# Kernel tuning notes

Hardware: AMD Instinct MI355X
Metric: run time of the kernel (lower is better)

## Reference

```python
import jax, jax.numpy as jnp
import numpy as np

B, S, H, NH = 2, 2048, 1024, 16
HD = H // NH


def setup_inputs() -> dict:
    key = jax.random.key(0)
    ks = jax.random.split(key, 14)
    lim = 1.0 / np.sqrt(H)  # torch Linear default init range
    def lin(ka, kb):
        W = jax.random.uniform(ka, (H, H), jnp.float32, -lim, lim)
        b = jax.random.uniform(kb, (H,), jnp.float32, -lim, lim)
        return W, b
    Wq, bq = lin(ks[0], ks[1])
    Wk, bk = lin(ks[2], ks[3])
    Wv, bv = lin(ks[4], ks[5])
    Wo, bo = lin(ks[6], ks[7])
    return {
        "query": jax.random.normal(ks[8], (B, S, H), jnp.float32),
        "key": jax.random.normal(ks[9], (B, S, H), jnp.float32),
        "value": jax.random.normal(ks[10], (B, S, H), jnp.float32),
        "attn_mask": jax.random.randint(ks[11], (B, S, S), 0, 2).astype(bool),
        "relative_time": jax.random.normal(ks[12], (B, 1, S, S), jnp.float32),
        "Wq": Wq, "bq": bq, "Wk": Wk, "bk": bk,
        "Wv": Wv, "bv": bv, "Wo": Wo, "bo": bo,
    }


def reference(query, key, value, attn_mask, relative_time,
              Wq, bq, Wk, bk, Wv, bv, Wo, bo):
    Bq, Sq, _ = query.shape
    Skv = key.shape[1]
    # projections (torch Linear: x @ W^T + b)
    Q = (query @ Wq.T + bq).reshape(Bq, Sq, NH, HD).transpose(0, 2, 1, 3)
    K = (key @ Wk.T + bk).reshape(Bq, Skv, NH, HD).transpose(0, 2, 1, 3)
    V = (value @ Wv.T + bv).reshape(Bq, Skv, NH, HD).transpose(0, 2, 1, 3)
    scale = HD ** (-0.5)
    # NOTE: bias added BEFORE scaling, matching the original (non-standard)
    scores = jnp.einsum("bhqd,bhkd->bhqk", Q, K)
    scores = (scores + relative_time) * scale
    scores = jnp.where(attn_mask[:, None, :, :], scores, -jnp.inf)
    attn = jax.nn.softmax(scores.astype(jnp.float32), axis=-1).astype(scores.dtype)
    attn = jnp.nan_to_num(attn, nan=0.0)
    # dropout is identity in eval mode (dropout_rate applied only when training)
    out = jnp.einsum("bhqk,bhkd->bhqd", attn, V)
    out = out.transpose(0, 2, 1, 3).reshape(Bq, Sq, H)
    return out @ Wo.T + bo
```

## Files before the change

### kernel.cpp

```cpp
#include <hip/hip_runtime.h>
#include <hip/hip_bf16.h>

constexpr int BATCH = 2, SEQ = 2048, HDIM = 1024, NHEADS = 16, HEADD = 64;
constexpr int MROWS = BATCH * SEQ;
constexpr float QSCALE = 0.18033688011112042f;

typedef short short8 __attribute__((ext_vector_type(8)));
typedef float f32x4  __attribute__((ext_vector_type(4)));

static __device__ __forceinline__ short f2bf(float f) {
    __hip_bfloat16 h = __float2bfloat16(f);
    return *reinterpret_cast<short*>(&h);
}

static __device__ __forceinline__ void gload_lds16(const void* g, void* l) {
    __builtin_amdgcn_global_load_lds(
        (const __attribute__((address_space(1))) unsigned int*)g,
        (__attribute__((address_space(3))) unsigned int*)l, 16, 0, 0);
}

__global__ void cvt_qkv_kernel(const float* __restrict__ q, const float* __restrict__ k,
                               const float* __restrict__ v, short* __restrict__ xq,
                               short* __restrict__ xk, short* __restrict__ xv, int n4) {
    int i = blockIdx.x * blockDim.x + threadIdx.x;
    const int stride = gridDim.x * blockDim.x;
    for (; i < 3 * n4; i += stride) {
        const float* in; short* out; int j = i;
        if (j >= 2 * n4)      { in = v; out = xv; j -= 2 * n4; }
        else if (j >= n4)     { in = k; out = xk; j -= n4; }
        else                  { in = q; out = xq; }
        const float4 val = reinterpret_cast<const float4*>(in)[j];
        short4 o;
        o.x = f2bf(val.x); o.y = f2bf(val.y); o.z = f2bf(val.z); o.w = f2bf(val.w);
        reinterpret_cast<short4*>(out)[j] = o;
    }
}

__global__ void cvt_w4_kernel(const float* __restrict__ w0, const float* __restrict__ w1,
                              const float* __restrict__ w2, const float* __restrict__ w3,
                              short* __restrict__ o0, short* __restrict__ o1,
                              short* __restrict__ o2, short* __restrict__ o3, int n4) {
    int i = blockIdx.x * blockDim.x + threadIdx.x;
    const int stride = gridDim.x * blockDim.x;
    for (; i < 4 * n4; i += stride) {
        const float* in; short* out; int j = i;
        if (j >= 3 * n4)      { in = w3; out = o3; j -= 3 * n4; }
        else if (j >= 2 * n4) { in = w2; out = o2; j -= 2 * n4; }
        else if (j >= n4)     { in = w1; out = o1; j -= n4; }
        else                  { in = w0; out = o0; }
        const float4 val = reinterpret_cast<const float4*>(in)[j];
        short4 o;
        o.x = f2bf(val.x); o.y = f2bf(val.y); o.z = f2bf(val.z); o.w = f2bf(val.w);
        reinterpret_cast<short4*>(out)[j] = o;
    }
}

__global__ void detect_mask_kernel(const unsigned int* __restrict__ m, int* flag) {
    const int tid = threadIdx.x;
    int gt1 = 0, isf = 0;
    for (int i = 0; i < 4; ++i) {
        unsigned int wv = m[tid + 256 * i];
        if (wv > 1u) gt1 = 1;
        if (wv == 0x3F800000u) isf = 1;
    }
    __shared__ int s_gt1, s_isf;
    if (tid == 0) { s_gt1 = 0; s_isf = 0; }
    __syncthreads();
    if (gt1) atomicOr(&s_gt1, 1);
    if (isf) atomicOr(&s_isf, 1);
    __syncthreads();
    if (tid == 0) flag[0] = s_gt1 ? (s_isf ? 2 : 1) : 0;
}

__global__ void fuse_rel_kernel(const float* __restrict__ rel, const void* __restrict__ mask,
                                const int* __restrict__ flag, float* __restrict__ relm,
                                int nPos) {
    const int f = flag[0];
    int i = blockIdx.x * blockDim.x + threadIdx.x;
    const int stride = gridDim.x * blockDim.x;
    for (; i < nPos; i += stride) {
        const int b  = i >> 20;
        const int qq = (i >> 11) & 511;
        const int k  = i & 2047;
        const long src = (((long)b * SEQ + qq * 4)) * SEQ + k;
        float4 o;
        float* op = reinterpret_cast<float*>(&o);
        for (int j = 0; j < 4; ++j) {
            const long s = src + (long)j * SEQ;
            const float v = rel[s];
            bool m;
            if (f == 0)      m = ((const int*)mask)[s] != 0;
            else if (f == 1) m = ((const unsigned char*)mask)[s] != 0;
            else             m = ((const float*)mask)[s] != 0.0f;
            op[j] = m ? v * QSCALE : -1e30f;
        }
        reinterpret_cast<float4*>(relm)[i] = o;
    }
}

template<typename EPI>
static __device__ __forceinline__
void gemm_core(const short* A, const short* Bw, int K, int m0, int n0, EPI epi) {
    __shared__ short As[128 * 64];
    __shared__ short Bs[128 * 64];
    const int tid  = threadIdx.x;
    const int lane = tid & 63;
    const int w    = tid >> 6;
    const int lo   = lane & 15, hi = lane >> 4;
    const int wm   = w >> 1, wn = w & 1;

    f32x4 acc[4][4] = {};

    const int arow = tid >> 3;
    const int acol = (tid & 7) * 8;
    const long aBase = (long)(m0 + arow) * K + acol;
    const long bBase = (long)(n0 + arow) * K + acol;

    for (int k0 = 0; k0 < K; k0 += 64) {
        for (int i = 0; i < 4; ++i) {
            gload_lds16(A  + aBase + (long)i * 32 * K + k0, (char*)As + i * 4096 + tid * 16);
            gload_lds16(Bw + bBase + (long)i * 32 * K + k0, (char*)Bs + i * 4096 + tid * 16);
        }
        __syncthreads();
        for (int ks = 0; ks < 2; ++ks) {
            short8 af[4], bf[4];
            const int koff = ks * 32 + hi * 8;
            for (int fm = 0; fm < 4; ++fm)
                af[fm] = *reinterpret_cast<const short8*>(&As[(wm * 64 + fm * 16 + lo) * 64 + koff]);
            for (int fn = 0; fn < 4; ++fn)
                bf[fn] = *reinterpret_cast<const short8*>(&Bs[(wn * 64 + fn * 16 + lo) * 64 + koff]);
            for (int fm = 0; fm < 4; ++fm)
                for (int fn = 0; fn < 4; ++fn)
                    acc[fm][fn] = __builtin_amdgcn_mfma_f32_16x16x32_bf16(
                        af[fm], bf[fn], acc[fm][fn], 0, 0, 0);
        }
        __syncthreads();
    }

    for (int fm = 0; fm < 4; ++fm)
        for (int fn = 0; fn < 4; ++fn) {
            const int n = n0 + wn * 64 + fn * 16 + lo;
            const int mB = m0 + wm * 64 + fm * 16 + hi * 4;
            for (int r = 0; r < 4; ++r) epi(mB + r, n, acc[fm][fn][r]);
        }
}

__global__ __launch_bounds__(256, 2)
void qkv_gemm(const short* xq, const short* xk, const short* xv,
              const short* wq, const short* wk, const short* wv,
              const float* bq, const float* bk, const float* bv,
              short* Qb, short* Kb, short* Vt) {
    const int which = blockIdx.x >> 8;
    const int bid   = blockIdx.x & 255;
    const int m0 = (bid >> 3) << 7;
    const int n0 = (bid & 7) << 7;
    const short* A    = which == 0 ? xq : which == 1 ? xk : xv;
    const short* W    = which == 0 ? wq : which == 1 ? wk : wv;
    const float* bias = which == 0 ? bq : which == 1 ? bk : bv;
    short* C          = which == 0 ? Qb : which == 1 ? Kb : Vt;
    const float scale = which == 0 ? QSCALE : 1.0f;
    gemm_core(A, W, HDIM, m0, n0, [&](int m, int n, float v) {
        v = (v + bias[n]) * scale;
        const int b = m >> 11, s = m & (SEQ - 1);
        const int h = n >> 6, d = n & 63;
        long idx;
        if (which != 2) idx = (((long)(b * NHEADS + h)) * SEQ + s) * HEADD + d;
        else            idx = (((long)(b * NHEADS + h)) * HEADD + d) * SEQ + s;
        C[idx] = f2bf(v);
    });
}

__global__ __launch_bounds__(256, 2)
void out_gemm(const short* A, const short* W, const float* bias,
              float* Cout) {
    const int bid = blockIdx.x;
    const int m0 = (bid >> 3) << 7;
    const int n0 = (bid & 7) << 7;
    gemm_core(A, W, HDIM, m0, n0, [&](int m, int n, float v) {
        Cout[(long)m * HDIM + n] = v + bias[n];
    });
}

__global__ __launch_bounds__(256, 4)
void attn_fwd(const short* __restrict__ Qb, const short* __restrict__ Kb,
              const short* __restrict__ Vtb, const float* __restrict__ relm,
              short* __restrict__ Ob) {
    __shared__ short Ks[2][64 * 64];
    __shared__ short Vs[2][64 * 64];
    __shared__ short Ps[4][16 * 64];
    const int tid  = threadIdx.x;
    const int lane = tid & 63;
    const int w    = tid >> 6;
    const int lo   = lane & 15, hi = lane >> 4;
    const int wg = ((blockIdx.x & 7) << 7) + (blockIdx.x >> 3);
    const int qt = wg & 31, h = (wg >> 5) & 15, b = wg >> 9;
    const int bh = b * NHEADS + h;

    short8 qf[2];
    {
        const long qbase = ((long)bh * SEQ + qt * 64 + w * 16 + lo) * HEADD;
        qf[0] = *reinterpret_cast<const short8*>(&Qb[qbase + hi * 8]);
        qf[1] = *reinterpret_cast<const short8*>(&Qb[qbase + 32 + hi * 8]);
    }

    float lsum[4] = {};
    f32x4 oacc[4] = {};

    const int srow  = tid >> 3;
    const int scolb = (tid & 7) * 16;
    const int scolK = scolb ^ ((srow & 7) << 4);
    const char* KbB = (const char*)Kb + ((long)bh * SEQ + srow) * 128 + scolK;
    const char* VbB = (const char*)Vtb + ((long)bh * HEADD + srow) * ((long)SEQ * 2) + scolK;

    auto stage = [&](int buf, int kt) {
        for (int i = 0; i < 2; ++i) {
            gload_lds16(KbB + ((long)kt * 64 + i * 32) * 128,
                        (char*)&Ks[buf][0] + i * 4096 + tid * 16);
            gload_lds16(VbB + (long)i * 32 * (SEQ * 2) + (long)kt * 128,
                        (char*)&Vs[buf][0] + i * 4096 + tid * 16);
        }
    };

    stage(0, 0);
    __syncthreads();

    const int rsw = (lo & 7) << 4;
    const f32x4* r4 = (const f32x4*)relm;
    const long rbase = ((long)b * 512 + qt * 16 + w * 4 + hi) * 2048 + lo;

    for (int kt = 0; kt < SEQ / 64; ++kt) {
        const int cb = kt & 1;
        if (kt < SEQ / 64 - 1) stage(cb ^ 1, kt + 1);

        f32x4 sc[4];
        for (int ct = 0; ct < 4; ++ct)
            sc[ct] = r4[rbase + kt * 64 + ct * 16];

        const char* kls = (const char*)&Ks[cb][0];
        for (int ct = 0; ct < 4; ++ct) {
            const int row = ct * 16 + lo;
            short8 kf0 = *(const short8*)(kls + row * 128 + ((hi * 16) ^ rsw));
            short8 kf1 = *(const short8*)(kls + row * 128 + ((64 + hi * 16) ^ rsw));
            sc[ct] = __builtin_amdgcn_mfma_f32_16x16x32_bf16(qf[0], kf0, sc[ct], 0, 0, 0);
            sc[ct] = __builtin_amdgcn_mfma_f32_16x16x32_bf16(qf[1], kf1, sc[ct], 0, 0, 0);
        }

        char* pls = (char*)&Ps[w][0];
        for (int ct = 0; ct < 4; ++ct)
            for (int r = 0; r < 4; ++r) {
                const float p = __builtin_amdgcn_exp2f(sc[ct][r]);
                lsum[r] += p;
                const int row = hi * 4 + r;
                *(short*)(pls + row * 128 + ((ct * 32 + lo * 2) ^ ((row & 7) << 4))) = f2bf(p);
            }

        short8 pf0 = *(const short8*)(pls + lo * 128 + ((hi * 16) ^ rsw));
        short8 pf1 = *(const short8*)(pls + lo * 128 + ((64 + hi * 16) ^ rsw));
        const char* vls = (const char*)&Vs[cb][0];
        for (int dt = 0; dt < 4; ++dt) {
            const int row = dt * 16 + lo;
            short8 vf0 = *(const short8*)(vls + row * 128 + ((hi * 16) ^ rsw));
            short8 vf1 = *(const short8*)(vls + row * 128 + ((64 + hi * 16) ^ rsw));
            oacc[dt] = __builtin_amdgcn_mfma_f32_16x16x32_bf16(pf0, vf0, oacc[dt], 0, 0, 0);
            oacc[dt] = __builtin_amdgcn_mfma_f32_16x16x32_bf16(pf1, vf1, oacc[dt], 0, 0, 0);
        }
        __syncthreads();
    }

    for (int r = 0; r < 4; ++r)
        for (int mk = 1; mk <= 8; mk <<= 1)
            lsum[r] += __shfl_xor(lsum[r], mk, 64);

    for (int r = 0; r < 4; ++r) {
        const int qg = qt * 64 + w * 16 + hi * 4 + r;
        const float inv = lsum[r] > 0.0f ? 1.0f / lsum[r] : 0.0f;
        for (int dt = 0; dt < 4; ++dt) {
            const int d = dt * 16 + lo;
            Ob[((long)b * SEQ + qg) * HDIM + h * 64 + d] = f2bf(oacc[dt][r] * inv);
        }
    }
}

extern "C" void kernel_launch(void* const* d_in, const int* in_sizes, int n_in,
                              void* d_out, int out_size, void* d_ws, size_t ws_size,
                              hipStream_t stream) {
    const float* q    = (const float*)d_in[0];
    const float* k    = (const float*)d_in[1];
    const float* v    = (const float*)d_in[2];
    const void*  mask = d_in[3];
    const float* rel  = (const float*)d_in[4];
    const float* Wq   = (const float*)d_in[5];
    const float* bq   = (const float*)d_in[6];
    const float* Wk   = (const float*)d_in[7];
    const float* bk   = (const float*)d_in[8];
    const float* Wv   = (const float*)d_in[9];
    const float* bv   = (const float*)d_in[10];
    const float* Wo   = (const float*)d_in[11];
    const float* bo   = (const float*)d_in[12];
    (void)in_sizes; (void)n_in; (void)out_size; (void)ws_size;

    char* ws = (char*)d_ws;
    size_t off = 0;
    auto alloc = [&](size_t bytes) {
        char* p = ws + off;
        off += (bytes + 255) & ~(size_t)255;
        return p;
    };
    const size_t xBytes = (size_t)MROWS * HDIM * 2;
    const size_t wBytes = (size_t)HDIM * HDIM * 2;
    const int    relPos = BATCH * 512 * 2048;
    const size_t relBytes = (size_t)relPos * 16;

    short* Qb  = (short*)alloc(xBytes);
    short* Kb  = (short*)alloc(xBytes);
    short* Vt  = (short*)alloc(xBytes);
    short* wob = (short*)alloc(wBytes);
    int*   flag = (int*)alloc(256);
    char* pool = (char*)alloc(relBytes);
    short* Ab  = (short*)alloc(xBytes);

    short* xq  = (short*)(pool);
    short* xk  = (short*)(pool + xBytes);
    short* xv  = (short*)(pool + 2 * xBytes);
    short* wqb = (short*)(pool + 3 * xBytes);
    short* wkb = (short*)(pool + 3 * xBytes + wBytes);
    short* wvb = (short*)(pool + 3 * xBytes + 2 * wBytes);
    float* relm = (float*)pool;

    const int n4x = MROWS * HDIM / 4, n4w = HDIM * HDIM / 4;
    cvt_qkv_kernel<<<1024, 256, 0, stream>>>(q, k, v, xq, xk, xv, n4x);
    cvt_w4_kernel<<<512, 256, 0, stream>>>(Wq, Wk, Wv, Wo, wqb, wkb, wvb, wob, n4w);
    detect_mask_kernel<<<1, 256, 0, stream>>>((const unsigned int*)mask, flag);

    qkv_gemm<<<768, 256, 0, stream>>>(xq, xk, xv, wqb, wkb, wvb,
                                      bq, bk, bv, Qb, Kb, Vt);

    fuse_rel_kernel<<<2048, 256, 0, stream>>>(rel, mask, flag, relm, relPos);

    attn_fwd<<<1024, 256, 0, stream>>>(Qb, Kb, Vt, relm, Ab);

    out_gemm<<<256, 256, 0, stream>>>(Ab, wob, bo, (float*)d_out);
}
```

Before: 185.7 us.

## Switch attention to 32x32 MFMA with register-resident P and bf16 bias

Result: faster. 168.9 us (-9.0%).

```diff
diff --git a/kernel.cpp b/kernel.cpp
--- a/kernel.cpp
+++ b/kernel.cpp
@@ -5,12 +5,25 @@
 constexpr int MROWS = BATCH * SEQ;
 constexpr float QSCALE = 0.18033688011112042f;
 
-typedef short short8 __attribute__((ext_vector_type(8)));
-typedef float f32x4  __attribute__((ext_vector_type(4)));
+typedef short short8  __attribute__((ext_vector_type(8)));
+typedef float f32x4   __attribute__((ext_vector_type(4)));
+typedef float f32x16  __attribute__((ext_vector_type(16)));
+typedef int   int4v   __attribute__((ext_vector_type(4)));
+typedef unsigned short ushort4v __attribute__((ext_vector_type(4)));
 
 static __device__ __forceinline__ short f2bf(float f) {
     __hip_bfloat16 h = __float2bfloat16(f);
     return *reinterpret_cast<short*>(&h);
+}
+
+static __device__ __forceinline__ int cvt_pk_bf16(float a, float b) {
+    int r;
+    asm("v_cvt_pk_bf16_f32 %0, %1, %2" : "=v"(r) : "v"(a), "v"(b));
+    return r;
+}
+
+static __device__ __forceinline__ float bfbits2f(unsigned short u) {
+    return __builtin_bit_cast(float, (unsigned int)u << 16);
 }
 
 static __device__ __forceinline__ void gload_lds16(const void* g, void* l) {
@@ -73,28 +86,50 @@
 }
 
 __global__ void fuse_rel_kernel(const float* __restrict__ rel, const void* __restrict__ mask,
-                                const int* __restrict__ flag, float* __restrict__ relm,
-                                int nPos) {
+                                const int* __restrict__ flag, short* __restrict__ rT,
+                                int nThr) {
     const int f = flag[0];
     int i = blockIdx.x * blockDim.x + threadIdx.x;
     const int stride = gridDim.x * blockDim.x;
-    for (; i < nPos; i += stride) {
-        const int b  = i >> 20;
-        const int qq = (i >> 11) & 511;
-        const int k  = i & 2047;
-        const long src = (((long)b * SEQ + qq * 4)) * SEQ + k;
-        float4 o;
-        float* op = reinterpret_cast<float*>(&o);
-        for (int j = 0; j < 4; ++j) {
-            const long s = src + (long)j * SEQ;
-            const float v = rel[s];
-            bool m;
-            if (f == 0)      m = ((const int*)mask)[s] != 0;
-            else if (f == 1) m = ((const unsigned char*)mask)[s] != 0;
-            else             m = ((const float*)mask)[s] != 0.0f;
-            op[j] = m ? v * QSCALE : -1e30f;
-        }
-        reinterpret_cast<float4*>(relm)[i] = o;
+    for (; i < nThr; i += stride) {
+        const int q    = i & 2047;
+        const int kv16 = (i >> 11) & 127;
+        const int b    = i >> 18;
+        const long base = ((long)(b * 2048 + q)) * 2048 + kv16 * 16;
+        float4 rv[4];
+        #pragma unroll
+        for (int g = 0; g < 4; ++g)
+            rv[g] = *reinterpret_cast<const float4*>(rel + base + 4 * g);
+        bool mk[16];
+        if (f == 1) {
+            const unsigned int* mp = (const unsigned int*)((const unsigned char*)mask + base);
+            #pragma unroll
+            for (int wd = 0; wd < 4; ++wd) {
+                const unsigned int mw = mp[wd];
+                #pragma unroll
+                for (int s = 0; s < 4; ++s) mk[wd * 4 + s] = ((mw >> (8 * s)) & 0xffu) != 0;
+            }
+        } else if (f == 0) {
+            const int* mp = (const int*)mask + base;
+            #pragma unroll
+            for (int j = 0; j < 16; ++j) mk[j] = mp[j] != 0;
+        } else {
+            const float* mp = (const float*)mask + base;
+            #pragma unroll
+            for (int j = 0; j < 16; ++j) mk[j] = mp[j] != 0.0f;
+        }
+        const float* rp = reinterpret_cast<const float*>(&rv[0]);
+        #pragma unroll
+        for (int g = 0; g < 4; ++g) {
+            short4 o;
+            short* op = reinterpret_cast<short*>(&o);
+            #pragma unroll
+            for (int j = 0; j < 4; ++j) {
+                const int idx = 4 * g + j;
+                op[j] = f2bf(mk[idx] ? rp[idx] * QSCALE : -1e30f);
+            }
+            *reinterpret_cast<short4*>(rT + (((long)(b * 512 + kv16 * 4 + g)) * 2048 + q) * 4) = o;
+        }
     }
 }
 
@@ -171,8 +206,7 @@
 }
 
 __global__ __launch_bounds__(256, 2)
-void out_gemm(const short* A, const short* W, const float* bias,
-              float* Cout) {
+void out_gemm(const short* A, const short* W, const float* bias, float* Cout) {
     const int bid = blockIdx.x;
     const int m0 = (bid >> 3) << 7;
     const int n0 = (bid & 7) << 7;
@@ -181,30 +215,31 @@
     });
 }
 
-__global__ __launch_bounds__(256, 4)
+__global__ __launch_bounds__(256, 2)
 void attn_fwd(const short* __restrict__ Qb, const short* __restrict__ Kb,
-              const short* __restrict__ Vtb, const float* __restrict__ relm,
+              const short* __restrict__ Vtb, const short* __restrict__ rT,
               short* __restrict__ Ob) {
     __shared__ short Ks[2][64 * 64];
     __shared__ short Vs[2][64 * 64];
-    __shared__ short Ps[4][16 * 64];
     const int tid  = threadIdx.x;
     const int lane = tid & 63;
-    const int w    = tid >> 6;
-    const int lo   = lane & 15, hi = lane >> 4;
-    const int wg = ((blockIdx.x & 7) << 7) + (blockIdx.x >> 3);
-    const int qt = wg & 31, h = (wg >> 5) & 15, b = wg >> 9;
+    const int wq   = tid >> 6;
+    const int l31  = lane & 31, hi2 = lane >> 5;
+    const int wg = ((blockIdx.x & 7) << 6) + (blockIdx.x >> 3);
+    const int qt = wg & 15, h = (wg >> 4) & 15, b = wg >> 8;
     const int bh = b * NHEADS + h;
-
-    short8 qf[2];
+    const int q0 = qt * 128 + wq * 32 + l31;
+
+    short8 qf[4];
     {
-        const long qbase = ((long)bh * SEQ + qt * 64 + w * 16 + lo) * HEADD;
-        qf[0] = *reinterpret_cast<const short8*>(&Qb[qbase + hi * 8]);
-        qf[1] = *reinterpret_cast<const short8*>(&Qb[qbase + 32 + hi * 8]);
-    }
-
-    float lsum[4] = {};
-    f32x4 oacc[4] = {};
+        const short* qp = Qb + ((long)bh * SEQ + q0) * HEADD + hi2 * 8;
+        #pragma unroll
+        for (int s = 0; s < 4; ++s)
+            qf[s] = *reinterpret_cast<const short8*>(qp + s * 16);
+    }
+
+    float lsum = 0.0f;
+    f32x16 oacc0 = {}, oacc1 = {};
 
     const int srow  = tid >> 3;
     const int scolb = (tid & 7) * 16;
@@ -213,6 +248,7 @@
     const char* VbB = (const char*)Vtb + ((long)bh * HEADD + srow) * ((long)SEQ * 2) + scolK;
 
     auto stage = [&](int buf, int kt) {
+        #pragma unroll
         for (int i = 0; i < 2; ++i) {
             gload_lds16(KbB + ((long)kt * 64 + i * 32) * 128,
                         (char*)&Ks[buf][0] + i * 4096 + tid * 16);
@@ -221,63 +257,105 @@
         }
     };
 
+    ushort4v rbuf[8];
+    auto loadRel = [&](int kt) {
+        #pragma unroll
+        for (int t = 0; t < 2; ++t)
+            #pragma unroll
+            for (int g = 0; g < 4; ++g) {
+                const int p4 = kt * 16 + t * 8 + 2 * g + hi2;
+                rbuf[t * 4 + g] = *reinterpret_cast<const ushort4v*>(
+                    rT + (((long)(b * 512 + p4)) * 2048 + q0) * 4);
+            }
+    };
+
     stage(0, 0);
+    loadRel(0);
     __syncthreads();
 
-    const int rsw = (lo & 7) << 4;
-    const f32x4* r4 = (const f32x4*)relm;
-    const long rbase = ((long)b * 512 + qt * 16 + w * 4 + hi) * 2048 + lo;
+    const int rsw = (l31 & 7) << 4;
 
     for (int kt = 0; kt < SEQ / 64; ++kt) {
         const int cb = kt & 1;
         if (kt < SEQ / 64 - 1) stage(cb ^ 1, kt + 1);
 
-        f32x4 sc[4];
-        for (int ct = 0; ct < 4; ++ct)
-            sc[ct] = r4[rbase + kt * 64 + ct * 16];
+        f32x16 sc[2];
+        #pragma unroll
+        for (int t = 0; t < 2; ++t)
+            #pragma unroll
+            for (int g = 0; g < 4; ++g)
+                #pragma unroll
+                for (int j = 0; j < 4; ++j)
+                    sc[t][4 * g + j] = bfbits2f(rbuf[t * 4 + g][j]);
+        loadRel(kt < SEQ / 64 - 1 ? kt + 1 : 0);
 
         const char* kls = (const char*)&Ks[cb][0];
-        for (int ct = 0; ct < 4; ++ct) {
-            const int row = ct * 16 + lo;
-            short8 kf0 = *(const short8*)(kls + row * 128 + ((hi * 16) ^ rsw));
-            short8 kf1 = *(const short8*)(kls + row * 128 + ((64 + hi * 16) ^ rsw));
-            sc[ct] = __builtin_amdgcn_mfma_f32_16x16x32_bf16(qf[0], kf0, sc[ct], 0, 0, 0);
-            sc[ct] = __builtin_amdgcn_mfma_f32_16x16x32_bf16(qf[1], kf1, sc[ct], 0, 0, 0);
-        }
-
-        char* pls = (char*)&Ps[w][0];
-        for (int ct = 0; ct < 4; ++ct)
-            for (int r = 0; r < 4; ++r) {
-                const float p = __builtin_amdgcn_exp2f(sc[ct][r]);
-                lsum[r] += p;
-                const int row = hi * 4 + r;
-                *(short*)(pls + row * 128 + ((ct * 32 + lo * 2) ^ ((row & 7) << 4))) = f2bf(p);
-            }
-
-        short8 pf0 = *(const short8*)(pls + lo * 128 + ((hi * 16) ^ rsw));
-        short8 pf1 = *(const short8*)(pls + lo * 128 + ((64 + hi * 16) ^ rsw));
+        __builtin_amdgcn_s_setprio(1);
+        #pragma unroll
+        for (int t = 0; t < 2; ++t) {
+            const char* kr = kls + (t * 32 + l31) * 128;
+            #pragma unroll
+            for (int s = 0; s < 4; ++s) {
+                short8 kf = *reinterpret_cast<const short8*>(kr + ((s * 32 + hi2 * 16) ^ rsw));
+                sc[t] = __builtin_amdgcn_mfma_f32_32x32x16_bf16(kf, qf[s], sc[t], 0, 0, 0);
+            }
+        }
+        __builtin_amdgcn_s_setprio(0);
+
+        int pa[4][4];
+        #pragma unroll
+        for (int t = 0; t < 2; ++t) {
+            int X[8];
+            #pragma unroll
+            for (int i2 = 0; i2 < 8; ++i2) {
+                const float p0 = __builtin_amdgcn_exp2f(sc[t][2 * i2]);
+                const float p1 = __builtin_amdgcn_exp2f(sc[t][2 * i2 + 1]);
+                lsum += p0 + p1;
+                X[i2] = cvt_pk_bf16(p0, p1);
+            }
+            #pragma unroll
+            for (int u = 0; u < 2; ++u) {
+                auto r0 = __builtin_amdgcn_permlane32_swap(X[4 * u + 0], X[4 * u + 2], false, false);
+                auto r1 = __builtin_amdgcn_permlane32_swap(X[4 * u + 1], X[4 * u + 3], false, false);
+                pa[2 * t + u][0] = (int)r0[0];
+                pa[2 * t + u][1] = (int)r1[0];
+                pa[2 * t + u][2] = (int)r0[1];
+                pa[2 * t + u][3] = (int)r1[1];
+            }
+        }
+
         const char* vls = (const char*)&Vs[cb][0];
-        for (int dt = 0; dt < 4; ++dt) {
-            const int row = dt * 16 + lo;
-            short8 vf0 = *(const short8*)(vls + row * 128 + ((hi * 16) ^ rsw));
-            short8 vf1 = *(const short8*)(vls + row * 128 + ((64 + hi * 16) ^ rsw));
-            oacc[dt] = __builtin_amdgcn_mfma_f32_16x16x32_bf16(pf0, vf0, oacc[dt], 0, 0, 0);
-            oacc[dt] = __builtin_amdgcn_mfma_f32_16x16x32_bf16(pf1, vf1, oacc[dt], 0, 0, 0);
-        }
+        __builtin_amdgcn_s_setprio(1);
+        #pragma unroll
+        for (int dt = 0; dt < 2; ++dt) {
+            const char* vr = vls + (dt * 32 + l31) * 128;
+            #pragma unroll
+            for (int s = 0; s < 4; ++s) {
+                short8 vf = *reinterpret_cast<const short8*>(vr + ((s * 32 + hi2 * 16) ^ rsw));
+                int4v pw = { pa[s][0], pa[s][1], pa[s][2], pa[s][3] };
+                if (dt == 0)
+                    oacc0 = __builtin_amdgcn_mfma_f32_32x32x16_bf16(
+                        __builtin_bit_cast(short8, pw), vf, oacc0, 0, 0, 0);
+                else
+                    oacc1 = __builtin_amdgcn_mfma_f32_32x32x16_bf16(
+                        __builtin_bit_cast(short8, pw), vf, oacc1, 0, 0, 0);
+            }
+        }
+        __builtin_amdgcn_s_setprio(0);
         __syncthreads();
     }
 
-    for (int r = 0; r < 4; ++r)
-        for (int mk = 1; mk <= 8; mk <<= 1)
-            lsum[r] += __shfl_xor(lsum[r], mk, 64);
-
-    for (int r = 0; r < 4; ++r) {
-        const int qg = qt * 64 + w * 16 + hi * 4 + r;
-        const float inv = lsum[r] > 0.0f ? 1.0f / lsum[r] : 0.0f;
-        for (int dt = 0; dt < 4; ++dt) {
-            const int d = dt * 16 + lo;
-            Ob[((long)b * SEQ + qg) * HDIM + h * 64 + d] = f2bf(oacc[dt][r] * inv);
-        }
+    lsum += __shfl_xor(lsum, 32, 64);
+    const float inv = lsum > 0.0f ? 1.0f / lsum : 0.0f;
+
+    #pragma unroll
+    for (int r = 0; r < 16; ++r) {
+        const int qloc = (r & 3) + 8 * (r >> 2) + 4 * hi2;
+        const float invr = __shfl(inv, qloc, 64);
+        const int qg = qt * 128 + wq * 32 + qloc;
+        const long obase = ((long)b * SEQ + qg) * HDIM + h * 64 + l31;
+        Ob[obase]      = f2bf(oacc0[r] * invr);
+        Ob[obase + 32] = f2bf(oacc1[r] * invr);
     }
 }
 
@@ -308,15 +386,14 @@
     };
     const size_t xBytes = (size_t)MROWS * HDIM * 2;
     const size_t wBytes = (size_t)HDIM * HDIM * 2;
-    const int    relPos = BATCH * 512 * 2048;
-    const size_t relBytes = (size_t)relPos * 16;
+    const size_t poolBytes = 3 * xBytes + 3 * wBytes;
 
     short* Qb  = (short*)alloc(xBytes);
     short* Kb  = (short*)alloc(xBytes);
     short* Vt  = (short*)alloc(xBytes);
     short* wob = (short*)alloc(wBytes);
     int*   flag = (int*)alloc(256);
-    char* pool = (char*)alloc(relBytes);
+    char* pool = (char*)alloc(poolBytes);
     short* Ab  = (short*)alloc(xBytes);
 
     short* xq  = (short*)(pool);
@@ -325,7 +402,7 @@
     short* wqb = (short*)(pool + 3 * xBytes);
     short* wkb = (short*)(pool + 3 * xBytes + wBytes);
     short* wvb = (short*)(pool + 3 * xBytes + 2 * wBytes);
-    float* relm = (float*)pool;
+    short* rT  = (short*)(pool);
 
     const int n4x = MROWS * HDIM / 4, n4w = HDIM * HDIM / 4;
     cvt_qkv_kernel<<<1024, 256, 0, stream>>>(q, k, v, xq, xk, xv, n4x);
@@ -335,9 +412,10 @@
     qkv_gemm<<<768, 256, 0, stream>>>(xq, xk, xv, wqb, wkb, wvb,
                                       bq, bk, bv, Qb, Kb, Vt);
 
-    fuse_rel_kernel<<<2048, 256, 0, stream>>>(rel, mask, flag, relm, relPos);
-
-    attn_fwd<<<1024, 256, 0, stream>>>(Qb, Kb, Vt, relm, Ab);
+    const int relThr = BATCH * 128 * 2048;
+    fuse_rel_kernel<<<2048, 256, 0, stream>>>(rel, mask, flag, rT, relThr);
+
+    attn_fwd<<<512, 256, 0, stream>>>(Qb, Kb, Vt, rT, Ab);
 
     out_gemm<<<256, 256, 0, stream>>>(Ab, wob, bo, (float*)d_out);
 }
```
